# Kernel tuning notes

Measured on AMD Instinct MI355X. Metric: run time of the kernel, lower is better.

The kernel has to match this reference:

```python
import jax, jax.numpy as jnp
import numpy as np

B, T, D, V = 2, 2048, 768, 50257
REWARD_SCALE = 0.5
DIV_WEIGHT = 0.1
EPS = 1e-8  # torch cosine_similarity eps


def setup_inputs() -> dict:
    key = jax.random.key(0)
    k1, k2, k3, k4 = jax.random.split(key, 4)
    return {
        "pass2_hidden": jax.random.normal(k1, (B, T, D), dtype=jnp.float32),
        "pass3_hidden": jax.random.normal(k2, (B, T, D), dtype=jnp.float32),
        "W": jax.random.normal(k3, (V, D), dtype=jnp.float32) * 0.02,  # lm_head weight [V, D]
        "targets": jax.random.randint(k4, (B, T), 0, V, dtype=jnp.int64),
    }


def _masked_ce(hidden, W, targets):
    # hidden: [B,T,D], W: [V,D], targets: [B,T] with ignore_index=-1
    logits = jnp.einsum('btd,vd->btv', hidden, W).reshape(B * T, V)
    t = targets.reshape(B * T)
    valid = t != -1
    safe_t = jnp.where(valid, t, 0)
    logp = jax.nn.log_softmax(logits, axis=-1)
    nll = -jnp.take_along_axis(logp, safe_t[:, None], axis=-1)[:, 0]
    nll = jnp.where(valid, nll, 0.0)
    return nll.sum() / jnp.maximum(valid.sum(), 1).astype(nll.dtype)


def reference(pass2_hidden, pass3_hidden, W, targets):
    # pass 2 CE computed under no_grad in the original
    loss_p2 = jax.lax.stop_gradient(_masked_ce(pass2_hidden, W, targets))
    loss_p3 = _masked_ce(pass3_hidden, W, targets)
    reward_loss = -REWARD_SCALE * (loss_p2 - loss_p3)

    p2 = jax.lax.stop_gradient(pass2_hidden.reshape(B * T, D))  # .detach()
    p3 = pass3_hidden.reshape(B * T, D)
    n2 = jnp.maximum(jnp.linalg.norm(p2, axis=-1), EPS)
    n3 = jnp.maximum(jnp.linalg.norm(p3, axis=-1), EPS)
    cos = jnp.sum(p2 * p3, axis=-1) / (n2 * n3)
    divergence_loss = DIV_WEIGHT * cos.mean()
    return reward_loss + divergence_loss
```

## Files before the change

### kernel.cpp

```cpp
#include <hip/hip_runtime.h>
#include <math.h>

#define BT     4096
#define M_TOT  8192
#define KDIM   768
#define VDIM   50257
#define NBLK   393
#define KCH    24
#define REWARD_SCALE 0.5
#define DIV_WEIGHT   0.1
#define EPS_COS      1e-8f
#define LOG2E        1.44269504088896340736f

typedef _Float16 half8 __attribute__((ext_vector_type(8)));
typedef float    f32x4 __attribute__((ext_vector_type(4)));

#define A_FRAGS (64*KCH*8*64)
#define W_FRAGS (NBLK*KCH*8*64)

__device__ __forceinline__ void g2l16(const short* g, short* l) {
    __builtin_amdgcn_global_load_lds(
        (const __attribute__((address_space(1))) unsigned int*)(const void*)g,
        (__attribute__((address_space(3))) unsigned int*)(void*)l,
        16, 0, 0);
}

__global__ __launch_bounds__(256)
void convert_A_kernel(const float* __restrict__ p2, const float* __restrict__ p3,
                      short* __restrict__ Ahi)
{
    __shared__ float Ls[128][36];
    const int mb = blockIdx.x;
    const int k0 = blockIdx.y;
    const int tid = threadIdx.x;

#pragma unroll
    for (int p = 0; p < 4; ++p) {
        int i = p * 1024 + tid * 4;
        int r = i >> 5;
        int c = i & 31;
        int m = mb * 128 + r;
        const float* src = (m < BT) ? (p2 + (size_t)m * KDIM)
                                    : (p3 + (size_t)(m - BT) * KDIM);
        float4 v = *(const float4*)(src + k0 * 32 + c);
        *(float4*)&Ls[r][c] = v;
    }
    __syncthreads();

    size_t base = ((size_t)(mb * KCH + k0) * 8) * 64;
#pragma unroll
    for (int h = 0; h < 2; ++h) {
        int f    = tid + h * 256;
        int lane = f & 63;
        int tile = f >> 6;
        int row  = tile * 16 + (lane & 15);
        int kq   = (lane >> 4) * 8;
        half8 out;
#pragma unroll
        for (int j = 0; j < 8; ++j) out[j] = (_Float16)Ls[row][kq + j];
        *(half8*)(Ahi + (base + f) * 8) = out;
    }
}

__global__ __launch_bounds__(256)
void convert_W_kernel(const float* __restrict__ W, short* __restrict__ Whi)
{
    __shared__ float Ls[128][36];
    const int nb = blockIdx.x;
    const int k0 = blockIdx.y;
    const int tid = threadIdx.x;

#pragma unroll
    for (int p = 0; p < 4; ++p) {
        int i = p * 1024 + tid * 4;
        int r = i >> 5;
        int c = i & 31;
        int v = nb * 128 + r;
        float4 val = make_float4(0.f, 0.f, 0.f, 0.f);
        if (v < VDIM) val = *(const float4*)(W + (size_t)v * KDIM + k0 * 32 + c);
        *(float4*)&Ls[r][c] = val;
    }
    __syncthreads();

    size_t base = ((size_t)(nb * KCH + k0) * 8) * 64;
#pragma unroll
    for (int h = 0; h < 2; ++h) {
        int f    = tid + h * 256;
        int lane = f & 63;
        int tile = f >> 6;
        int row  = tile * 16 + (lane & 15);
        int kq   = (lane >> 4) * 8;
        half8 out;
#pragma unroll
        for (int j = 0; j < 8; ++j) out[j] = (_Float16)(Ls[row][kq + j] * LOG2E);
        *(half8*)(Whi + (base + f) * 8) = out;
    }
}

__global__ __launch_bounds__(256, 4)
void gemm_f16_kernel(const short* __restrict__ Ahi, const short* __restrict__ Whi,
                     double* __restrict__ g_sumexp)
{
    __shared__ __align__(16) short As[2][8][64][8];
    __shared__ float rowsum[128];

    const int tid    = threadIdx.x;
    const int lane   = tid & 63;
    const int wave   = tid >> 6;
    const int wave_m = wave >> 1;
    const int wave_n = wave & 1;
    const int mb = blockIdx.x;
    const int nb = blockIdx.y;

    if (tid < 128) rowsum[tid] = 0.0f;

    f32x4 acc[4][4];
#pragma unroll
    for (int i = 0; i < 4; ++i)
#pragma unroll
        for (int j = 0; j < 4; ++j) acc[i][j] = (f32x4)0.0f;

    const short* Ablk  = Ahi + (size_t)mb * KCH * 4096 + lane * 8;
    const short* Bbase = Whi + (size_t)nb * KCH * 4096
                             + ((size_t)(wave_n * 4) * 64 + lane) * 8;

#define STAGEA(k0_, buf_)                                                     \
    {                                                                         \
        _Pragma("unroll")                                                     \
        for (int j = 0; j < 2; ++j) {                                         \
            int c = wave * 2 + j;                                             \
            g2l16(Ablk + (size_t)((k0_) * 8 + c) * 512, &As[buf_][c][lane][0]);\
        }                                                                     \
    }

    half8 b[2][4];
    STAGEA(0, 0);
#pragma unroll
    for (int tn = 0; tn < 4; ++tn)
        b[0][tn] = *(const half8*)(Bbase + tn * 512);

#pragma unroll 2
    for (int k0 = 0; k0 < KCH; ++k0) {
        const int buf = k0 & 1;
        __syncthreads();
        if (k0 + 1 < KCH) {
            STAGEA(k0 + 1, buf ^ 1);
#pragma unroll
            for (int tn = 0; tn < 4; ++tn)
                b[buf ^ 1][tn] = *(const half8*)(Bbase + (size_t)(k0 + 1) * 4096
                                                 + tn * 512);
        }
        half8 a[4];
#pragma unroll
        for (int tm = 0; tm < 4; ++tm)
            a[tm] = *(const half8*)&As[buf][wave_m * 4 + tm][lane][0];
#pragma unroll
        for (int tm = 0; tm < 4; ++tm)
#pragma unroll
            for (int tn = 0; tn < 4; ++tn)
                acc[tm][tn] = __builtin_amdgcn_mfma_f32_16x16x32_f16(
                                  a[tm], b[buf][tn], acc[tm][tn], 0, 0, 0);
    }
#undef STAGEA

    __syncthreads();
    const int colBase = nb * 128 + wave_n * 64;
    const int quad = lane >> 4;
    const int cidx = lane & 15;
#pragma unroll
    for (int tm = 0; tm < 4; ++tm) {
#pragma unroll
        for (int r = 0; r < 4; ++r) {
            float s = 0.0f;
#pragma unroll
            for (int tn = 0; tn < 4; ++tn) {
                int col = colBase + tn * 16 + cidx;
                if (col < VDIM) s += __builtin_amdgcn_exp2f(acc[tm][tn][r]);
            }
            s += __shfl_xor(s, 1);
            s += __shfl_xor(s, 2);
            s += __shfl_xor(s, 4);
            s += __shfl_xor(s, 8);
            if (cidx == 0) {
                int row = wave_m * 64 + tm * 16 + quad * 4 + r;
                atomicAdd(&rowsum[row], s);
            }
        }
    }
    __syncthreads();
    if (tid < 128) {
        atomicAdd(&g_sumexp[(size_t)mb * 128 + tid], (double)rowsum[tid]);
    }
}

#define BM 128
#define BN 128
#define BK 16
#define LDPAD 4
__global__ __launch_bounds__(256)
void logits_expsum_kernel(const float* __restrict__ p2,
                          const float* __restrict__ p3,
                          const float* __restrict__ W,
                          double* __restrict__ g_sumexp)
{
    __shared__ float As[BK][BM + LDPAD];
    __shared__ float Bsh[BK][BN + LDPAD];
    __shared__ float rowsum[BM];

    const int tid     = threadIdx.x;
    const int rowBase = blockIdx.y * BM;
    const int colBase = blockIdx.x * BN;

    if (tid < BM) rowsum[tid] = 0.0f;

    float acc[8][8];
#pragma unroll
    for (int i = 0; i < 8; ++i)
#pragma unroll
        for (int j = 0; j < 8; ++j) acc[i][j] = 0.0f;

    const int ty = tid >> 4;
    const int tx = tid & 15;
    const int r0 = ty * 8;
    const int c0 = tx * 4;

    for (int k0 = 0; k0 < KDIM; k0 += BK) {
        __syncthreads();
#pragma unroll
        for (int l = 0; l < 2; ++l) {
            int id  = tid + l * 256;
            int row = id >> 2;
            int kq  = id & 3;
            int m   = rowBase + row;
            const float* src = (m < BT) ? (p2 + (size_t)m * KDIM)
                                        : (p3 + (size_t)(m - BT) * KDIM);
            float4 v = *(const float4*)(src + k0 + kq * 4);
            As[kq * 4 + 0][row] = v.x;
            As[kq * 4 + 1][row] = v.y;
            As[kq * 4 + 2][row] = v.z;
            As[kq * 4 + 3][row] = v.w;
        }
#pragma unroll
        for (int l = 0; l < 2; ++l) {
            int id  = tid + l * 256;
            int row = id >> 2;
            int kq  = id & 3;
            int c   = colBase + row;
            int cs  = (c < VDIM) ? c : (VDIM - 1);
            float4 v = *(const float4*)(W + (size_t)cs * KDIM + k0 + kq * 4);
            Bsh[kq * 4 + 0][row] = v.x;
            Bsh[kq * 4 + 1][row] = v.y;
            Bsh[kq * 4 + 2][row] = v.z;
            Bsh[kq * 4 + 3][row] = v.w;
        }
        __syncthreads();
#pragma unroll
        for (int kk = 0; kk < BK; ++kk) {
            float a[8], bb[8];
            *(float4*)&a[0]  = *(const float4*)&As[kk][r0];
            *(float4*)&a[4]  = *(const float4*)&As[kk][r0 + 4];
            *(float4*)&bb[0] = *(const float4*)&Bsh[kk][c0];
            *(float4*)&bb[4] = *(const float4*)&Bsh[kk][64 + c0];
#pragma unroll
            for (int i = 0; i < 8; ++i)
#pragma unroll
                for (int j = 0; j < 8; ++j)
                    acc[i][j] = fmaf(a[i], bb[j], acc[i][j]);
        }
    }

    __syncthreads();
#pragma unroll
    for (int i = 0; i < 8; ++i) {
        float s = 0.0f;
#pragma unroll
        for (int j = 0; j < 8; ++j) {
            int c = colBase + ((j < 4) ? (c0 + j) : (64 + c0 + (j - 4)));
            if (c < VDIM) s += expf(acc[i][j]);
        }
        atomicAdd(&rowsum[r0 + i], s);
    }
    __syncthreads();
    if (tid < BM) {
        atomicAdd(&g_sumexp[rowBase + tid], (double)rowsum[tid]);
    }
}

__global__ __launch_bounds__(256)
void finalize_tokens_kernel(const float* __restrict__ p2,
                            const float* __restrict__ p3,
                            const float* __restrict__ W,
                            const int*   __restrict__ targets,
                            const double* __restrict__ g_sumexp,
                            double* __restrict__ tokvals)
{
    const int t   = blockIdx.x;
    const int tid = threadIdx.x;
    const int tg  = targets[t];
    const bool valid = (tg >= 0);
    const float* w = W + (size_t)(valid ? tg : 0) * KDIM;
    const float* a = p2 + (size_t)t * KDIM;
    const float* b = p3 + (size_t)t * KDIM;

    float s22 = 0.f, s33 = 0.f, s23 = 0.f, s2w = 0.f, s3w = 0.f;
    for (int i = tid; i < KDIM; i += 256) {
        float x = a[i], y = b[i], ww = w[i];
        s22 = fmaf(x, x, s22);
        s33 = fmaf(y, y, s33);
        s23 = fmaf(x, y, s23);
        s2w = fmaf(x, ww, s2w);
        s3w = fmaf(y, ww, s3w);
    }
#pragma unroll
    for (int off = 32; off > 0; off >>= 1) {
        s22 += __shfl_down(s22, off);
        s33 += __shfl_down(s33, off);
        s23 += __shfl_down(s23, off);
        s2w += __shfl_down(s2w, off);
        s3w += __shfl_down(s3w, off);
    }
    __shared__ float sm[5][4];
    const int wv = tid >> 6, lane = tid & 63;
    if (lane == 0) {
        sm[0][wv] = s22; sm[1][wv] = s33; sm[2][wv] = s23;
        sm[3][wv] = s2w; sm[4][wv] = s3w;
    }
    __syncthreads();
    if (tid == 0) {
        float S22 = sm[0][0] + sm[0][1] + sm[0][2] + sm[0][3];
        float S33 = sm[1][0] + sm[1][1] + sm[1][2] + sm[1][3];
        float S23 = sm[2][0] + sm[2][1] + sm[2][2] + sm[2][3];
        float S2w = sm[3][0] + sm[3][1] + sm[3][2] + sm[3][3];
        float S3w = sm[4][0] + sm[4][1] + sm[4][2] + sm[4][3];

        float n2 = fmaxf(sqrtf(S22), EPS_COS);
        float n3 = fmaxf(sqrtf(S33), EPS_COS);

        double4 out;
        out.x = valid ? (log(g_sumexp[t])      - (double)S2w) : 0.0;
        out.y = valid ? (log(g_sumexp[BT + t]) - (double)S3w) : 0.0;
        out.z = (double)(S23 / (n2 * n3));
        out.w = valid ? 1.0 : 0.0;
        *(double4*)(tokvals + 4 * (size_t)t) = out;
    }
}

__global__ __launch_bounds__(1024)
void final_scalar_kernel(const double* __restrict__ tokvals,
                         float* __restrict__ out)
{
    const int tid = threadIdx.x;
    double s0 = 0.0, s1 = 0.0, s2 = 0.0, s3 = 0.0;
    for (int t = tid; t < BT; t += 1024) {
        double4 v = *(const double4*)(tokvals + 4 * (size_t)t);
        s0 += v.x; s1 += v.y; s2 += v.z; s3 += v.w;
    }
#pragma unroll
    for (int off = 32; off > 0; off >>= 1) {
        s0 += __shfl_down(s0, off);
        s1 += __shfl_down(s1, off);
        s2 += __shfl_down(s2, off);
        s3 += __shfl_down(s3, off);
    }
    __shared__ double sm[4][16];
    const int wv = tid >> 6, lane = tid & 63;
    if (lane == 0) { sm[0][wv] = s0; sm[1][wv] = s1; sm[2][wv] = s2; sm[3][wv] = s3; }
    __syncthreads();
    if (tid == 0) {
        double S0 = 0, S1 = 0, S2 = 0, S3 = 0;
#pragma unroll
        for (int i = 0; i < 16; ++i) { S0 += sm[0][i]; S1 += sm[1][i]; S2 += sm[2][i]; S3 += sm[3][i]; }
        double cnt = (S3 > 0.0) ? S3 : 1.0;
        double loss_p2 = S0 / cnt;
        double loss_p3 = S1 / cnt;
        double reward_loss = -REWARD_SCALE * (loss_p2 - loss_p3);
        double divergence  =  DIV_WEIGHT * (S2 / (double)BT);
        out[0] = (float)(reward_loss + divergence);
    }
}

extern "C" void kernel_launch(void* const* d_in, const int* in_sizes, int n_in,
                              void* d_out, int out_size, void* d_ws, size_t ws_size,
                              hipStream_t stream)
{
    const float* p2  = (const float*)d_in[0];
    const float* p3  = (const float*)d_in[1];
    const float* W   = (const float*)d_in[2];
    const int*   tgt = (const int*)d_in[3];

    double* g_sumexp = (double*)d_ws;
    double* tokvals  = g_sumexp + M_TOT;
    char*   fragbase = (char*)d_ws + 196608;

    hipMemsetAsync(d_ws, 0, 65536, stream);

    const size_t need = 196608 + (size_t)A_FRAGS * 16 + (size_t)W_FRAGS * 16;
    if (ws_size >= need) {
        short* Ahi = (short*)fragbase;
        short* Whi = Ahi + (size_t)A_FRAGS * 8;

        convert_A_kernel<<<dim3(64, KCH), dim3(256), 0, stream>>>(p2, p3, Ahi);
        convert_W_kernel<<<dim3(NBLK, KCH), dim3(256), 0, stream>>>(W, Whi);
        gemm_f16_kernel<<<dim3(64, NBLK), dim3(256), 0, stream>>>(Ahi, Whi, g_sumexp);
    } else {
        logits_expsum_kernel<<<dim3(NBLK, 64), dim3(256), 0, stream>>>(p2, p3, W, g_sumexp);
    }

    finalize_tokens_kernel<<<dim3(BT), dim3(256), 0, stream>>>(
        p2, p3, W, tgt, g_sumexp, tokvals);

    final_scalar_kernel<<<dim3(1), dim3(1024), 0, stream>>>(tokvals, (float*)d_out);
}
```

Baseline: 876.6 us.

## Enlarge f16 GEMM tiles to 256x256 with LDS-staged A and B pipeline

Rewrites the logits/exp-sum GEMM to use 512-thread blocks computing 256x256 output tiles, with both A and W fragments streamed into double-buffered LDS through global_load_lds. Previously W fragments were loaded straight into registers per wave. Each wave now holds an 8x4 grid of MFMA accumulators. The main loop uses hand-placed s_barrier and vmcnt waits, sched_barrier and setprio around the MFMA bursts, so loads overlap compute. The aim is higher arithmetic intensity per byte loaded and fewer blocks, at the cost of more registers and LDS per block, lower occupancy, and fragile manual synchronisation.

Measured after the change: 925.7 us. 1.06x slower.

```diff
diff --git a/kernel.cpp b/kernel.cpp
--- a/kernel.cpp
+++ b/kernel.cpp
@@ -6,7 +6,9 @@
 #define KDIM   768
 #define VDIM   50257
 #define NBLK   393
+#define NB256  197
 #define KCH    24
+#define KT     12
 #define REWARD_SCALE 0.5
 #define DIV_WEIGHT   0.1
 #define EPS_COS      1e-8f
@@ -97,99 +99,162 @@
     }
 }
 
-__global__ __launch_bounds__(256, 4)
+#define BARRIER()  asm volatile("s_barrier" ::: "memory")
+#define WAITV(n_)  asm volatile("s_waitcnt vmcnt(" #n_ ")" ::: "memory")
+#define SB0()      __builtin_amdgcn_sched_barrier(0)
+
+__global__ __launch_bounds__(512, 2)
 void gemm_f16_kernel(const short* __restrict__ Ahi, const short* __restrict__ Whi,
                      double* __restrict__ g_sumexp)
 {
-    __shared__ __align__(16) short As[2][8][64][8];
-    __shared__ float rowsum[128];
-
-    const int tid    = threadIdx.x;
-    const int lane   = tid & 63;
-    const int wave   = tid >> 6;
-    const int wave_m = wave >> 1;
-    const int wave_n = wave & 1;
-    const int mb = blockIdx.x;
-    const int nb = blockIdx.y;
-
-    if (tid < 128) rowsum[tid] = 0.0f;
-
-    f32x4 acc[4][4];
-#pragma unroll
-    for (int i = 0; i < 4; ++i)
+    __shared__ __align__(16) short As[2][32][64][8];
+    __shared__ __align__(16) short Bs[2][32][64][8];
+
+    const int tid  = threadIdx.x;
+    const int lane = tid & 63;
+    const int w    = tid >> 6;
+    const int wm   = w >> 2;
+    const int wn   = w & 3;
+    const int mb   = blockIdx.x;
+    const int nb   = blockIdx.y;
+
+    const int  f0       = (w & 3) * 4;
+    const int  sh       = f0 >> 3;
+    const int  tileBase = f0 & 7;
+    const bool isB      = (w >= 4);
+    const int  nb128    = min(2 * nb + sh, NBLK - 1);
+    const short* gbase  = isB
+        ? Whi + (size_t)nb128 * KCH * 4096 + lane * 8
+        : Ahi + (size_t)(2 * mb + sh) * KCH * 4096 + lane * 8;
+    short* stageL = (isB ? &Bs[0][0][0][0] : &As[0][0][0][0])
+                    + lane * 8 + f0 * 512;
+
+#define STAGEH(kc_, bufn_)                                                    \
+    {                                                                         \
+        short* l0 = stageL + ((bufn_) * 32 + ((kc_) & 1) * 16) * 512;         \
+        const short* g0 = gbase + (size_t)((kc_) * 8 + tileBase) * 512;       \
+        _Pragma("unroll")                                                     \
+        for (int j = 0; j < 4; ++j) g2l16(g0 + j * 512, l0 + j * 512);        \
+    }
+
+    const short* aRd = &As[0][wm * 8][lane][0];
+    const short* bRd = &Bs[0][(wn >> 1) * 8 + (wn & 1) * 4][lane][0];
+#define RDA(CUR_, kh_, mh_, i_) \
+    (*(const half8*)(aRd + ((CUR_) * 32 + (kh_) * 16 + (mh_) * 4 + (i_)) * 512))
+#define RDB(CUR_, kh_, i_) \
+    (*(const half8*)(bRd + ((CUR_) * 32 + (kh_) * 16 + (i_)) * 512))
+
+    f32x4 acc[8][4];
+#pragma unroll
+    for (int i = 0; i < 8; ++i)
 #pragma unroll
         for (int j = 0; j < 4; ++j) acc[i][j] = (f32x4)0.0f;
 
-    const short* Ablk  = Ahi + (size_t)mb * KCH * 4096 + lane * 8;
-    const short* Bbase = Whi + (size_t)nb * KCH * 4096
-                             + ((size_t)(wave_n * 4) * 64 + lane) * 8;
-
-#define STAGEA(k0_, buf_)                                                     \
+#define MFMA16(mh_)                                                           \
+    __builtin_amdgcn_s_setprio(1);                                            \
+    _Pragma("unroll")                                                         \
+    for (int mt = 0; mt < 4; ++mt)                                            \
+        _Pragma("unroll")                                                     \
+        for (int nt = 0; nt < 4; ++nt)                                        \
+            acc[(mh_) * 4 + mt][nt] = __builtin_amdgcn_mfma_f32_16x16x32_f16( \
+                a[mt], b[nt], acc[(mh_) * 4 + mt][nt], 0, 0, 0);              \
+    __builtin_amdgcn_s_setprio(0);
+
+#define KTILE(kt_, CUR_, STG_, LAST_)                                         \
     {                                                                         \
-        _Pragma("unroll")                                                     \
-        for (int j = 0; j < 2; ++j) {                                         \
-            int c = wave * 2 + j;                                             \
-            g2l16(Ablk + (size_t)((k0_) * 8 + c) * 512, &As[buf_][c][lane][0]);\
+        half8 a[4], b[4];                                                     \
+                  \
+        if (STG_) {                                                           \
+            STAGEH(2 * ((kt_) + 1), (CUR_) ^ 1);                              \
+            SB0();                                                            \
+            STAGEH(2 * ((kt_) + 1) + 1, (CUR_) ^ 1);                          \
         }                                                                     \
-    }
-
-    half8 b[2][4];
-    STAGEA(0, 0);
-#pragma unroll
-    for (int tn = 0; tn < 4; ++tn)
-        b[0][tn] = *(const half8*)(Bbase + tn * 512);
-
-#pragma unroll 2
-    for (int k0 = 0; k0 < KCH; ++k0) {
-        const int buf = k0 & 1;
-        __syncthreads();
-        if (k0 + 1 < KCH) {
-            STAGEA(k0 + 1, buf ^ 1);
-#pragma unroll
-            for (int tn = 0; tn < 4; ++tn)
-                b[buf ^ 1][tn] = *(const half8*)(Bbase + (size_t)(k0 + 1) * 4096
-                                                 + tn * 512);
-        }
-        half8 a[4];
-#pragma unroll
-        for (int tm = 0; tm < 4; ++tm)
-            a[tm] = *(const half8*)&As[buf][wave_m * 4 + tm][lane][0];
-#pragma unroll
-        for (int tm = 0; tm < 4; ++tm)
-#pragma unroll
-            for (int tn = 0; tn < 4; ++tn)
-                acc[tm][tn] = __builtin_amdgcn_mfma_f32_16x16x32_f16(
-                                  a[tm], b[buf][tn], acc[tm][tn], 0, 0, 0);
-    }
-#undef STAGEA
-
-    __syncthreads();
-    const int colBase = nb * 128 + wave_n * 64;
+        _Pragma("unroll")                                                     \
+        for (int i = 0; i < 4; ++i) {                                         \
+            a[i] = RDA(CUR_, 0, 0, i);                                        \
+            b[i] = RDB(CUR_, 0, i);                                           \
+        }                                                                     \
+        BARRIER(); SB0();                                                     \
+        MFMA16(0);                                                            \
+        SB0(); BARRIER();                                                     \
+                                                                      \
+        _Pragma("unroll")                                                     \
+        for (int i = 0; i < 4; ++i) a[i] = RDA(CUR_, 0, 1, i);                \
+        BARRIER(); SB0();                                                     \
+        MFMA16(1);                                                            \
+        SB0();                                                                \
+        if (LAST_) { WAITV(0); } else { WAITV(8); }                           \
+        BARRIER();                                                            \
+                                                                      \
+        _Pragma("unroll")                                                     \
+        for (int i = 0; i < 4; ++i) {                                         \
+            a[i] = RDA(CUR_, 1, 0, i);                                        \
+            b[i] = RDB(CUR_, 1, i);                                           \
+        }                                                                     \
+        BARRIER(); SB0();                                                     \
+        MFMA16(0);                                                            \
+        SB0(); BARRIER();                                                     \
+                                                                      \
+        _Pragma("unroll")                                                     \
+        for (int i = 0; i < 4; ++i) a[i] = RDA(CUR_, 1, 1, i);                \
+        BARRIER(); SB0();                                                     \
+        MFMA16(1);                                                            \
+        SB0();                                                                \
+        if (!(LAST_)) { WAITV(4); }                                           \
+        BARRIER();                                                            \
+    }
+
+    STAGEH(0, 0);
+    SB0();
+    STAGEH(1, 0);
+    WAITV(4);
+    BARRIER();
+
+#pragma unroll 1
+    for (int kt = 0; kt < 10; kt += 2) {
+        KTILE(kt,     0, 1, 0)
+        KTILE(kt + 1, 1, 1, 0)
+    }
+    KTILE(10, 0, 1, 0)
+    KTILE(11, 1, 0, 1)
+
+#undef KTILE
+#undef MFMA16
+#undef RDA
+#undef RDB
+#undef STAGEH
+
+    __syncthreads();
+    float* rowsum = (float*)&As[0][0][0][0];
+    if (tid < 256) rowsum[tid] = 0.0f;
+    __syncthreads();
+
+    const int colBase = nb * 256 + wn * 64;
     const int quad = lane >> 4;
     const int cidx = lane & 15;
 #pragma unroll
-    for (int tm = 0; tm < 4; ++tm) {
+    for (int mt = 0; mt < 8; ++mt) {
 #pragma unroll
         for (int r = 0; r < 4; ++r) {
             float s = 0.0f;
 #pragma unroll
-            for (int tn = 0; tn < 4; ++tn) {
-                int col = colBase + tn * 16 + cidx;
-                if (col < VDIM) s += __builtin_amdgcn_exp2f(acc[tm][tn][r]);
+            for (int nt = 0; nt < 4; ++nt) {
+                int col = colBase + nt * 16 + cidx;
+                if (col < VDIM) s += __builtin_amdgcn_exp2f(acc[mt][nt][r]);
             }
             s += __shfl_xor(s, 1);
             s += __shfl_xor(s, 2);
             s += __shfl_xor(s, 4);
             s += __shfl_xor(s, 8);
             if (cidx == 0) {
-                int row = wave_m * 64 + tm * 16 + quad * 4 + r;
+                int row = wm * 128 + mt * 16 + quad * 4 + r;
                 atomicAdd(&rowsum[row], s);
             }
         }
     }
     __syncthreads();
-    if (tid < 128) {
-        atomicAdd(&g_sumexp[(size_t)mb * 128 + tid], (double)rowsum[tid]);
+    if (tid < 256) {
+        atomicAdd(&g_sumexp[(size_t)mb * 256 + tid], (double)rowsum[tid]);
     }
 }
 
@@ -401,7 +466,7 @@
 
         convert_A_kernel<<<dim3(64, KCH), dim3(256), 0, stream>>>(p2, p3, Ahi);
         convert_W_kernel<<<dim3(NBLK, KCH), dim3(256), 0, stream>>>(W, Whi);
-        gemm_f16_kernel<<<dim3(64, NBLK), dim3(256), 0, stream>>>(Ahi, Whi, g_sumexp);
+        gemm_f16_kernel<<<dim3(32, NB256), dim3(512), 0, stream>>>(Ahi, Whi, g_sumexp);
     } else {
         logits_expsum_kernel<<<dim3(NBLK, 64), dim3(256), 0, stream>>>(p2, p3, W, g_sumexp);
     }
```
